# Kernel tuning notes

Hardware: AMD Instinct MI355X
Metric: run time of the kernel (lower is better)

Reference implementation:

```python
import jax, jax.numpy as jnp
import numpy as np


def setup_inputs() -> dict:
    key = jax.random.key(0)
    x = jax.random.normal(key, (4, 4, 32, 256, 256), dtype=jnp.float32)
    return {"x": x}


def reference(x):
    # NonMaximaSuppression3d with kernel_size=(3,3,3) fast path:
    # a voxel survives iff it is strictly greater than all 26 neighbors;
    # border voxels (no full neighborhood) are always suppressed.
    B, CH, D, H, W = x.shape
    ct = x[..., 1:-1, 1:-1, 1:-1]  # interior centers [B,CH,D-2,H-2,W-2]
    mask_inner = jnp.ones(ct.shape, dtype=bool)
    for dz in range(3):
        for dy in range(3):
            for dx in range(3):
                if (dz, dy, dx) == (1, 1, 1):
                    continue
                neigh = x[..., dz:D - 2 + dz, dy:H - 2 + dy, dx:W - 2 + dx]
                mask_inner = mask_inner & (ct > neigh)
    mask = jnp.zeros(x.shape, dtype=bool).at[..., 1:-1, 1:-1, 1:-1].set(mask_inner)
    return x * mask.astype(x.dtype)
```

## Files before the change

kernel.cpp:

```cpp
#include <hip/hip_runtime.h>


typedef float v4f __attribute__((ext_vector_type(4)));

constexpr int W  = 256;
constexpr int H  = 256;
constexpr int D  = 32;
constexpr int SH = W;
constexpr int SD = W * H;
constexpr int KD = 4;
constexpr int HC = 8;
constexpr int BC = 16;
constexpr int DG = D / KD;
constexpr int HG = H / HC;
constexpr int NPL = KD + 2;
constexpr int NR  = HC + 2;
constexpr int TROWS = NPL * NR;

__device__ __forceinline__ v4f vmax4(v4f a, v4f b) {
    return (v4f){fmaxf(a.x, b.x), fmaxf(a.y, b.y), fmaxf(a.z, b.z), fmaxf(a.w, b.w)};
}

__global__ __launch_bounds__(256) void nms3d_kernel(const float* __restrict__ x,
                                                    float* __restrict__ out) {
    __shared__ float lds[TROWS * W];

    const int blk  = blockIdx.x;
    const int wv   = threadIdx.x >> 6;
    const int lane = threadIdx.x & 63;
    const int hc   = blk & (HG - 1);
    const int dg   = (blk >> 5) & (DG - 1);
    const int bc   = blk >> 8;
    const int d0   = dg * KD;
    const int h0   = hc * HC;

    const float* vol = x + bc * (D * SD);

    #pragma unroll
    for (int u = 0; u < TROWS / 4; ++u) {
        const int t = wv * (TROWS / 4) + u;
        const int j = t / NR;
        const int r = t - j * NR;
        int p = d0 - 1 + j;  p = p < 0 ? 0 : (p > D - 1 ? D - 1 : p);
        int hh = h0 - 1 + r; hh = hh < 0 ? 0 : (hh > H - 1 ? H - 1 : hh);
        const float* gp = vol + p * SD + hh * SH + (lane << 2);
        __builtin_amdgcn_global_load_lds(
            (const __attribute__((address_space(1))) unsigned int*)gp,
            (__attribute__((address_space(3))) unsigned int*)&lds[(j * NR + r) * W],
            16, 0, 0);
    }
    __syncthreads();

    const int d = d0 + wv;
    const bool dv = (d > 0) && (d < D - 1);
    float* ovol = out + bc * (D * SD) + d * SD + (lane << 2);

    const float* Lm = lds + (wv * NR) * W + (lane << 2);
    const float* L0 = lds + ((wv + 1) * NR) * W + (lane << 2);
    const float* Lp = lds + ((wv + 2) * NR) * W + (lane << 2);

    v4f rm[3], r0[3], rp[3];
    rm[0] = *(const v4f*)(Lm + 0 * W); r0[0] = *(const v4f*)(L0 + 0 * W); rp[0] = *(const v4f*)(Lp + 0 * W);
    rm[1] = *(const v4f*)(Lm + 1 * W); r0[1] = *(const v4f*)(L0 + 1 * W); rp[1] = *(const v4f*)(Lp + 1 * W);

    #pragma unroll
    for (int i = 0; i < HC; ++i) {
        const int s0 = i % 3, s1 = (i + 1) % 3, s2 = (i + 2) % 3;
        rm[s2] = *(const v4f*)(Lm + (i + 2) * W);
        r0[s2] = *(const v4f*)(L0 + (i + 2) * W);
        rp[s2] = *(const v4f*)(Lp + (i + 2) * W);

        const v4f a3m = vmax4(vmax4(rm[s0], rm[s1]), rm[s2]);
        const v4f a3p = vmax4(vmax4(rp[s0], rp[s1]), rp[s2]);
        const v4f a20 = vmax4(r0[s0], r0[s2]);
        const v4f v8  = vmax4(vmax4(a3m, a3p), a20);
        const v4f c   = r0[s1];

        const float l8 = __shfl_up(v8.w, 1);
        const float r8 = __shfl_down(v8.x, 1);
        const float lc = __shfl_up(c.w, 1);
        const float rc = __shfl_down(c.x, 1);

        float n0 = fmaxf(fmaxf(l8,   v8.x), v8.y);
        float n1 = fmaxf(fmaxf(v8.x, v8.y), v8.z);
        float n2 = fmaxf(fmaxf(v8.y, v8.z), v8.w);
        float n3 = fmaxf(fmaxf(v8.z, v8.w), r8);
        n0 = fmaxf(n0, fmaxf(lc,  c.y));
        n1 = fmaxf(n1, fmaxf(c.x, c.z));
        n2 = fmaxf(n2, fmaxf(c.y, c.w));
        n3 = fmaxf(n3, fmaxf(c.z, rc));

        const int h = h0 + i;
        const bool hv = (h > 0) && (h < H - 1);
        const bool v  = hv && dv;
        v4f o;
        o.x = (v && lane > 0  && c.x > n0) ? c.x : 0.f;
        o.y = (v && c.y > n1) ? c.y : 0.f;
        o.z = (v && c.z > n2) ? c.z : 0.f;
        o.w = (v && lane < 63 && c.w > n3) ? c.w : 0.f;
        __builtin_nontemporal_store(o, (v4f*)(ovol + h * SH));
    }
}

extern "C" void kernel_launch(void* const* d_in, const int* in_sizes, int n_in,
                              void* d_out, int out_size, void* d_ws, size_t ws_size,
                              hipStream_t stream) {
    const float* x = (const float*)d_in[0];
    float* out = (float*)d_out;
    const int grid = BC * DG * HG;
    nms3d_kernel<<<grid, 256, 0, stream>>>(x, out);
}
```

Measured before the change: 226.1 us.

## Stream depth planes through a 4-slot LDS ring buffer with prefetch

Each block now walks half the depth (16 planes) of one 8-row tile, keeping a rotating 4-plane LDS ring. It prefetches plane d+2 while computing plane d, and each wave handles two output rows. This cuts the depth halo re-reads from 6/4 planes per output plane to about 1, and overlaps loads with compute. The cost is a __syncthreads per plane, a much smaller grid (1024 blocks instead of 4096), and serial per-block latency that may limit memory-level parallelism.

Result: slower. 241.6 us (+6.9%).

```diff
diff --git a/kernel.cpp b/kernel.cpp
--- a/kernel.cpp
+++ b/kernel.cpp
@@ -8,97 +8,126 @@
 constexpr int D  = 32;
 constexpr int SH = W;
 constexpr int SD = W * H;
-constexpr int KD = 4;
 constexpr int HC = 8;
+constexpr int NR = HC + 2;
+constexpr int NSLOT = 4;
 constexpr int BC = 16;
-constexpr int DG = D / KD;
 constexpr int HG = H / HC;
-constexpr int NPL = KD + 2;
-constexpr int NR  = HC + 2;
-constexpr int TROWS = NPL * NR;
+constexpr int SPLIT = 2;
+constexpr int DR = D / SPLIT;
+constexpr int PLW = NR * W;
 
 __device__ __forceinline__ v4f vmax4(v4f a, v4f b) {
     return (v4f){fmaxf(a.x, b.x), fmaxf(a.y, b.y), fmaxf(a.z, b.z), fmaxf(a.w, b.w)};
 }
 
-__global__ __launch_bounds__(256) void nms3d_kernel(const float* __restrict__ x,
-                                                    float* __restrict__ out) {
-    __shared__ float lds[TROWS * W];
+__device__ __forceinline__ void stage_plane(const float* __restrict__ vol,
+                                            float* lds, int p, int h0,
+                                            int wv, int lane) {
+    const int pc = p < 0 ? 0 : (p > D - 1 ? D - 1 : p);
+    float* dst = lds + (p & 3) * PLW;
+    const float* src = vol + pc * SD + (lane << 2);
+    {
+        int hh = h0 - 1 + wv; hh = hh < 0 ? 0 : hh;
+        __builtin_amdgcn_global_load_lds(
+            (const __attribute__((address_space(1))) unsigned int*)(src + hh * SH),
+            (__attribute__((address_space(3))) unsigned int*)(dst + wv * W), 16, 0, 0);
+    }
+    {
+        const int hh = h0 - 1 + wv + 4;
+        __builtin_amdgcn_global_load_lds(
+            (const __attribute__((address_space(1))) unsigned int*)(src + hh * SH),
+            (__attribute__((address_space(3))) unsigned int*)(dst + (wv + 4) * W), 16, 0, 0);
+    }
+    if (wv < 2) {
+        int hh = h0 - 1 + wv + 8; hh = hh > H - 1 ? H - 1 : hh;
+        __builtin_amdgcn_global_load_lds(
+            (const __attribute__((address_space(1))) unsigned int*)(src + hh * SH),
+            (__attribute__((address_space(3))) unsigned int*)(dst + (wv + 8) * W), 16, 0, 0);
+    }
+}
+
+__device__ __forceinline__ v4f nms_row(v4f m0, v4f m1, v4f m2,
+                                       v4f c0, v4f c1, v4f c2,
+                                       v4f p0, v4f p1, v4f p2,
+                                       bool valid, int lane) {
+    const v4f a3m = vmax4(vmax4(m0, m1), m2);
+    const v4f a3p = vmax4(vmax4(p0, p1), p2);
+    const v4f a20 = vmax4(c0, c2);
+    const v4f v8  = vmax4(vmax4(a3m, a3p), a20);
+    const v4f c   = c1;
+
+    const float l8 = __shfl_up(v8.w, 1);
+    const float r8 = __shfl_down(v8.x, 1);
+    const float lc = __shfl_up(c.w, 1);
+    const float rc = __shfl_down(c.x, 1);
+
+    float n0 = fmaxf(fmaxf(l8,   v8.x), v8.y);
+    float n1 = fmaxf(fmaxf(v8.x, v8.y), v8.z);
+    float n2 = fmaxf(fmaxf(v8.y, v8.z), v8.w);
+    float n3 = fmaxf(fmaxf(v8.z, v8.w), r8);
+    n0 = fmaxf(n0, fmaxf(lc,  c.y));
+    n1 = fmaxf(n1, fmaxf(c.x, c.z));
+    n2 = fmaxf(n2, fmaxf(c.y, c.w));
+    n3 = fmaxf(n3, fmaxf(c.z, rc));
+
+    v4f o;
+    o.x = (valid && lane > 0  && c.x > n0) ? c.x : 0.f;
+    o.y = (valid && c.y > n1) ? c.y : 0.f;
+    o.z = (valid && c.z > n2) ? c.z : 0.f;
+    o.w = (valid && lane < 63 && c.w > n3) ? c.w : 0.f;
+    return o;
+}
+
+__global__ __launch_bounds__(256, 4) void nms3d_kernel(const float* __restrict__ x,
+                                                       float* __restrict__ out) {
+    __shared__ float lds[NSLOT * PLW];
 
     const int blk  = blockIdx.x;
     const int wv   = threadIdx.x >> 6;
     const int lane = threadIdx.x & 63;
     const int hc   = blk & (HG - 1);
-    const int dg   = (blk >> 5) & (DG - 1);
-    const int bc   = blk >> 8;
-    const int d0   = dg * KD;
+    const int half = (blk >> 5) & (SPLIT - 1);
+    const int bc   = blk >> 6;
+    const int d0   = half * DR;
     const int h0   = hc * HC;
 
-    const float* vol = x + bc * (D * SD);
+    const float* vol  = x   + bc * (D * SD);
+    float*       ovol = out + bc * (D * SD);
 
-    #pragma unroll
-    for (int u = 0; u < TROWS / 4; ++u) {
-        const int t = wv * (TROWS / 4) + u;
-        const int j = t / NR;
-        const int r = t - j * NR;
-        int p = d0 - 1 + j;  p = p < 0 ? 0 : (p > D - 1 ? D - 1 : p);
-        int hh = h0 - 1 + r; hh = hh < 0 ? 0 : (hh > H - 1 ? H - 1 : hh);
-        const float* gp = vol + p * SD + hh * SH + (lane << 2);
-        __builtin_amdgcn_global_load_lds(
-            (const __attribute__((address_space(1))) unsigned int*)gp,
-            (__attribute__((address_space(3))) unsigned int*)&lds[(j * NR + r) * W],
-            16, 0, 0);
-    }
+    stage_plane(vol, lds, d0 - 1, h0, wv, lane);
+    stage_plane(vol, lds, d0,     h0, wv, lane);
+    stage_plane(vol, lds, d0 + 1, h0, wv, lane);
     __syncthreads();
 
-    const int d = d0 + wv;
-    const bool dv = (d > 0) && (d < D - 1);
-    float* ovol = out + bc * (D * SD) + d * SD + (lane << 2);
+    const int i0 = wv * 2;
+    const int h  = h0 + i0;
+    const bool hv0 = (h > 0) && (h < H - 1);
+    const bool hv1 = (h + 1 < H - 1);
 
-    const float* Lm = lds + (wv * NR) * W + (lane << 2);
-    const float* L0 = lds + ((wv + 1) * NR) * W + (lane << 2);
-    const float* Lp = lds + ((wv + 2) * NR) * W + (lane << 2);
+    #pragma unroll 1
+    for (int d = d0; d < d0 + DR; ++d) {
+        stage_plane(vol, lds, d + 2, h0, wv, lane);
 
-    v4f rm[3], r0[3], rp[3];
-    rm[0] = *(const v4f*)(Lm + 0 * W); r0[0] = *(const v4f*)(L0 + 0 * W); rp[0] = *(const v4f*)(Lp + 0 * W);
-    rm[1] = *(const v4f*)(Lm + 1 * W); r0[1] = *(const v4f*)(L0 + 1 * W); rp[1] = *(const v4f*)(Lp + 1 * W);
+        const bool dv = (d > 0) && (d < D - 1);
+        const float* Lm = lds + ((d - 1) & 3) * PLW + i0 * W + (lane << 2);
+        const float* L0 = lds + ( d      & 3) * PLW + i0 * W + (lane << 2);
+        const float* Lp = lds + ((d + 1) & 3) * PLW + i0 * W + (lane << 2);
 
-    #pragma unroll
-    for (int i = 0; i < HC; ++i) {
-        const int s0 = i % 3, s1 = (i + 1) % 3, s2 = (i + 2) % 3;
-        rm[s2] = *(const v4f*)(Lm + (i + 2) * W);
-        r0[s2] = *(const v4f*)(L0 + (i + 2) * W);
-        rp[s2] = *(const v4f*)(Lp + (i + 2) * W);
+        const v4f m0 = *(const v4f*)(Lm + 0 * W), m1 = *(const v4f*)(Lm + 1 * W);
+        const v4f m2 = *(const v4f*)(Lm + 2 * W), m3 = *(const v4f*)(Lm + 3 * W);
+        const v4f c0 = *(const v4f*)(L0 + 0 * W), c1 = *(const v4f*)(L0 + 1 * W);
+        const v4f c2 = *(const v4f*)(L0 + 2 * W), c3 = *(const v4f*)(L0 + 3 * W);
+        const v4f p0 = *(const v4f*)(Lp + 0 * W), p1 = *(const v4f*)(Lp + 1 * W);
+        const v4f p2 = *(const v4f*)(Lp + 2 * W), p3 = *(const v4f*)(Lp + 3 * W);
 
-        const v4f a3m = vmax4(vmax4(rm[s0], rm[s1]), rm[s2]);
-        const v4f a3p = vmax4(vmax4(rp[s0], rp[s1]), rp[s2]);
-        const v4f a20 = vmax4(r0[s0], r0[s2]);
-        const v4f v8  = vmax4(vmax4(a3m, a3p), a20);
-        const v4f c   = r0[s1];
+        float* orow = ovol + d * SD + h * SH + (lane << 2);
+        const v4f o0 = nms_row(m0, m1, m2, c0, c1, c2, p0, p1, p2, hv0 && dv, lane);
+        __builtin_nontemporal_store(o0, (v4f*)orow);
+        const v4f o1 = nms_row(m1, m2, m3, c1, c2, c3, p1, p2, p3, hv1 && dv, lane);
+        __builtin_nontemporal_store(o1, (v4f*)(orow + SH));
 
-        const float l8 = __shfl_up(v8.w, 1);
-        const float r8 = __shfl_down(v8.x, 1);
-        const float lc = __shfl_up(c.w, 1);
-        const float rc = __shfl_down(c.x, 1);
-
-        float n0 = fmaxf(fmaxf(l8,   v8.x), v8.y);
-        float n1 = fmaxf(fmaxf(v8.x, v8.y), v8.z);
-        float n2 = fmaxf(fmaxf(v8.y, v8.z), v8.w);
-        float n3 = fmaxf(fmaxf(v8.z, v8.w), r8);
-        n0 = fmaxf(n0, fmaxf(lc,  c.y));
-        n1 = fmaxf(n1, fmaxf(c.x, c.z));
-        n2 = fmaxf(n2, fmaxf(c.y, c.w));
-        n3 = fmaxf(n3, fmaxf(c.z, rc));
-
-        const int h = h0 + i;
-        const bool hv = (h > 0) && (h < H - 1);
-        const bool v  = hv && dv;
-        v4f o;
-        o.x = (v && lane > 0  && c.x > n0) ? c.x : 0.f;
-        o.y = (v && c.y > n1) ? c.y : 0.f;
-        o.z = (v && c.z > n2) ? c.z : 0.f;
-        o.w = (v && lane < 63 && c.w > n3) ? c.w : 0.f;
-        __builtin_nontemporal_store(o, (v4f*)(ovol + h * SH));
+        __syncthreads();
     }
 }
 
@@ -107,6 +136,6 @@
                               hipStream_t stream) {
     const float* x = (const float*)d_in[0];
     float* out = (float*)d_out;
-    const int grid = BC * DG * HG;
+    const int grid = BC * HG * SPLIT;
     nms3d_kernel<<<grid, 256, 0, stream>>>(x, out);
 }
```

## Split LDS tile loads into two phases to overlap compute with loads

Applied to the files above, without the earlier changes.

The tile load is now issued in two groups: rows 0-5 of every plane first, then rows 6-9. Each group is followed by a partial vmcnt wait and a barrier. The first four output rows are computed once the first group lands, and the wait for the remaining rows is deferred to iteration 4, which hides part of the global-to-LDS latency behind compute. The vmcnt counts rely on the outstanding store count, so the schedule is fragile. Launch bounds also gain a minimum of two blocks per SM.

Result: no change. 225.3 us (-0.4%).

```diff
diff --git a/kernel.cpp b/kernel.cpp
--- a/kernel.cpp
+++ b/kernel.cpp
@@ -15,15 +15,14 @@
 constexpr int HG = H / HC;
 constexpr int NPL = KD + 2;
 constexpr int NR  = HC + 2;
-constexpr int TROWS = NPL * NR;
 
 __device__ __forceinline__ v4f vmax4(v4f a, v4f b) {
     return (v4f){fmaxf(a.x, b.x), fmaxf(a.y, b.y), fmaxf(a.z, b.z), fmaxf(a.w, b.w)};
 }
 
-__global__ __launch_bounds__(256) void nms3d_kernel(const float* __restrict__ x,
-                                                    float* __restrict__ out) {
-    __shared__ float lds[TROWS * W];
+__global__ __launch_bounds__(256, 2) void nms3d_kernel(const float* __restrict__ x,
+                                                       float* __restrict__ out) {
+    __shared__ float lds[NPL * NR * W];
 
     const int blk  = blockIdx.x;
     const int wv   = threadIdx.x >> 6;
@@ -37,10 +36,10 @@
     const float* vol = x + bc * (D * SD);
 
     #pragma unroll
-    for (int u = 0; u < TROWS / 4; ++u) {
-        const int t = wv * (TROWS / 4) + u;
-        const int j = t / NR;
-        const int r = t - j * NR;
+    for (int u = 0; u < 9; ++u) {
+        const int t = wv * 9 + u;
+        const int j = t / 6;
+        const int r = t - j * 6;
         int p = d0 - 1 + j;  p = p < 0 ? 0 : (p > D - 1 ? D - 1 : p);
         int hh = h0 - 1 + r; hh = hh < 0 ? 0 : (hh > H - 1 ? H - 1 : hh);
         const float* gp = vol + p * SD + hh * SH + (lane << 2);
@@ -49,7 +48,23 @@
             (__attribute__((address_space(3))) unsigned int*)&lds[(j * NR + r) * W],
             16, 0, 0);
     }
-    __syncthreads();
+    #pragma unroll
+    for (int u = 0; u < 6; ++u) {
+        const int t = wv * 6 + u;
+        const int j = t / 4;
+        const int r = 6 + (t - j * 4);
+        int p = d0 - 1 + j;  p = p < 0 ? 0 : (p > D - 1 ? D - 1 : p);
+        int hh = h0 - 1 + r; hh = hh > H - 1 ? H - 1 : hh;
+        const float* gp = vol + p * SD + hh * SH + (lane << 2);
+        __builtin_amdgcn_global_load_lds(
+            (const __attribute__((address_space(1))) unsigned int*)gp,
+            (__attribute__((address_space(3))) unsigned int*)&lds[(j * NR + r) * W],
+            16, 0, 0);
+    }
+    __builtin_amdgcn_sched_barrier(0);
+    asm volatile("s_waitcnt vmcnt(6)" ::: "memory");
+    __builtin_amdgcn_s_barrier();
+    __builtin_amdgcn_sched_barrier(0);
 
     const int d = d0 + wv;
     const bool dv = (d > 0) && (d < D - 1);
@@ -65,6 +80,12 @@
 
     #pragma unroll
     for (int i = 0; i < HC; ++i) {
+        if (i == 4) {
+            __builtin_amdgcn_sched_barrier(0);
+            asm volatile("s_waitcnt vmcnt(4)" ::: "memory");
+            __builtin_amdgcn_s_barrier();
+            __builtin_amdgcn_sched_barrier(0);
+        }
         const int s0 = i % 3, s1 = (i + 1) % 3, s2 = (i + 2) % 3;
         rm[s2] = *(const v4f*)(Lm + (i + 2) * W);
         r0[s2] = *(const v4f*)(L0 + (i + 2) * W);
```
